# Kernel tuning notes

Hardware: AMD Instinct MI355X
Metric: run time of the kernel (lower is better)

## Reference

```python
import jax, jax.numpy as jnp
import numpy as np

B, N, T, F, D = 2, 8, 128, 128, 256
EPS = 1e-5


def setup_inputs() -> dict:
    key = jax.random.key(0)
    ks = jax.random.split(key, 8)
    s = 1.0 / np.sqrt(D)
    s2 = 1.0 / np.sqrt(2 * D)
    return {
        "x": jax.random.normal(ks[0], (B, N, D), dtype=jnp.float32),
        "t_emb": jax.random.normal(ks[1], (T, D), dtype=jnp.float32),
        "f_emb": jax.random.normal(ks[2], (F, D), dtype=jnp.float32),
        "ln_g": jnp.ones((D,), dtype=jnp.float32),
        "ln_b": jnp.zeros((D,), dtype=jnp.float32),
        "W1": jax.random.uniform(ks[3], (D, 2 * D), jnp.float32, -s, s),
        "b1": jax.random.uniform(ks[4], (2 * D,), jnp.float32, -s, s),
        "W2": jax.random.uniform(ks[5], (2 * D, 2), jnp.float32, -s2, s2),
        "b2": jax.random.uniform(ks[6], (2,), jnp.float32, -s2, s2),
    }


def reference(x, t_emb, f_emb, ln_g, ln_b, W1, b1, W2, b2):
    # x: [B,N,D]; pos_emb: [T,F,D]; broadcast-add -> [B,N,T,F,D]
    pos = t_emb[:, None, :] + f_emb[None, :, :]            # [T,F,D]
    h = x[:, :, None, None, :] + pos[None, None]           # [B,N,T,F,D]
    # LayerNorm over last dim
    mu = jnp.mean(h, axis=-1, keepdims=True)
    var = jnp.mean(jnp.square(h - mu), axis=-1, keepdims=True)
    h = (h - mu) * jax.lax.rsqrt(var + EPS) * ln_g + ln_b
    # MLP: D -> 2D -> 2
    h = jax.nn.relu(jnp.einsum("bntfd,de->bntfe", h, W1) + b1)
    out = jnp.einsum("bntfe,eo->bntfo", h, W2) + b2        # [B,N,T,F,2]
    return out
```

## Files before the change

kernel.cpp:

```cpp
#include <hip/hip_runtime.h>
#include <stdint.h>


#define D_ 256
#define E_ 512

typedef __attribute__((ext_vector_type(8))) short short8;
typedef __attribute__((ext_vector_type(4))) short short4v;
typedef __attribute__((ext_vector_type(4))) float f32x4;
typedef __attribute__((ext_vector_type(2))) float f32x2;

__device__ alignas(16) unsigned short g_Abuf[2176 * 768];
__device__ alignas(16) unsigned short g_Bbuf[768 * 640];
__device__ alignas(16) float g_U[2048 * 512];
__device__ alignas(16) float g_C[2048 * 128];
__device__ alignas(16) float g_Vt[512 * 128];
__device__ alignas(16) float g_GKW[512 * 4];
__device__ alignas(16) float g_sxt[2048];
__device__ alignas(16) float g_sqxt[2048];
__device__ alignas(16) float g_sf[128];
__device__ alignas(16) float g_sqf[128];

__device__ inline unsigned short f2bf(float f) {
  unsigned int u = __float_as_uint(f);
  u += 0x7fffu + ((u >> 16) & 1u);
  return (unsigned short)(u >> 16);
}
__device__ inline float bf2f(unsigned short h) {
  return __uint_as_float(((unsigned int)h) << 16);
}

__global__ __launch_bounds__(256) void prep(
    const float* __restrict__ x, const float* __restrict__ t_emb,
    const float* __restrict__ f_emb, const float* __restrict__ ln_g,
    const float* __restrict__ ln_b, const float* __restrict__ W1,
    const float* __restrict__ b1, const float* __restrict__ W2) {
  __shared__ float sW[32][264];
  __shared__ float sF[128][36];
  __shared__ float sg[32];
  __shared__ float red[4][64][2];

  const int blk = blockIdx.x;
  const int tid = threadIdx.x;
  const int wv = tid >> 6;
  const int l = tid & 63;

  if (blk < 544) {
    int arow;
    float v0, v1, v2, v3;
    if (blk < 512) {
      const int r = blk * 4 + wv;
      const int bn = r >> 7, t = r & 127;
      const float4 xv = *(const float4*)(x + bn * D_ + 4 * l);
      const float4 tv = *(const float4*)(t_emb + t * D_ + 4 * l);
      v0 = xv.x + tv.x; v1 = xv.y + tv.y;
      v2 = xv.z + tv.z; v3 = xv.w + tv.w;
      arow = r;
    } else {
      const int fi = (blk - 512) * 4 + wv;
      const float4 fv = *(const float4*)(f_emb + fi * D_ + 4 * l);
      v0 = fv.x; v1 = fv.y; v2 = fv.z; v3 = fv.w;
      arow = 2048 + fi;
    }
    union { unsigned short u[4]; short4v v; } hi, lo;
    hi.u[0] = f2bf(v0); hi.u[1] = f2bf(v1);
    hi.u[2] = f2bf(v2); hi.u[3] = f2bf(v3);
    lo.u[0] = f2bf(v0 - bf2f(hi.u[0]));
    lo.u[1] = f2bf(v1 - bf2f(hi.u[1]));
    lo.u[2] = f2bf(v2 - bf2f(hi.u[2]));
    lo.u[3] = f2bf(v3 - bf2f(hi.u[3]));
    unsigned short* ab = g_Abuf + arow * 768 + 4 * l;
    *(short4v*)(ab) = hi.v;
    *(short4v*)(ab + 256) = lo.v;
    *(short4v*)(ab + 512) = hi.v;
    float s = (v0 + v1) + (v2 + v3);
    float q = fmaf(v0, v0, fmaf(v1, v1, fmaf(v2, v2, v3 * v3)));
#pragma unroll
    for (int d = 1; d < 64; d <<= 1) {
      s += __shfl_xor(s, d);
      q += __shfl_xor(q, d);
    }
    if (l == 0) {
      if (arow < 2048) { g_sxt[arow] = s; g_sqxt[arow] = q; }
      else             { g_sf[arow - 2048] = s; g_sqf[arow - 2048] = q; }
    }
  } else if (blk < 552) {
    const int e = (blk - 544) * 64 + l;
    const int k0 = wv * 64;
    float G = 0.f, K = 0.f;
#pragma unroll 8
    for (int i = 0; i < 64; ++i) {
      const float wval = W1[(k0 + i) * E_ + e];
      G = fmaf(ln_g[k0 + i], wval, G);
      K = fmaf(ln_b[k0 + i], wval, K);
    }
    red[wv][l][0] = G;
    red[wv][l][1] = K;
    __syncthreads();
    if (wv == 0) {
      G = (red[0][l][0] + red[1][l][0]) + (red[2][l][0] + red[3][l][0]);
      K = (red[0][l][1] + red[1][l][1]) + (red[2][l][1] + red[3][l][1]);
      float4 o;
      o.x = G; o.y = K + b1[e];
      o.z = W2[2 * e]; o.w = W2[2 * e + 1];
      *(float4*)(g_GKW + 4 * e) = o;
    }
  } else {
    const int b = blk - 552;
    const int kt = b >> 1, h = b & 1;
    const int term = kt >> 3;
    const int k0 = (kt & 7) * 32;
    {
      const float4* w4 = (const float4*)(W1 + (size_t)k0 * E_ + h * 256);
      for (int i = tid; i < 2048; i += 256) {
        const int kk2 = i >> 6, c4 = i & 63;
        *(float4*)&sW[kk2][c4 * 4] = w4[kk2 * (E_ / 4) + c4];
      }
      if (tid < 32) sg[tid] = ln_g[k0 + tid];
      if (h == 0) {
        const float4* f4 = (const float4*)(f_emb + k0);
        for (int i = tid; i < 1024; i += 256) {
          const int fr = i >> 3, c4 = i & 7;
          *(float4*)&sF[fr][c4 * 4] = f4[fr * (D_ / 4) + c4];
        }
      }
    }
    __syncthreads();
    for (int fi = tid; fi < 1024; fi += 256) {
      const int ct = 4 * h + (fi >> 8);
      const int rem = fi & 255;
      const int jtl = rem >> 6, ln = rem & 63;
      const int colw = (ct - 4 * h) * 64 + jtl * 16 + (ln & 15);
      const int kb = ((ln >> 4) & 3) * 8;
      union { unsigned short u[8]; short8 v; } fr8;
#pragma unroll
      for (int j = 0; j < 8; ++j) {
        const float v = sg[kb + j] * sW[kb + j][colw];
        const unsigned short hv = f2bf(v);
        fr8.u[j] = (term == 2) ? f2bf(v - bf2f(hv)) : hv;
      }
      const int gidx = ((kt * 10 + ct) * 4 + jtl) * 64 + ln;
      *(short8*)(g_Bbuf + gidx * 8) = fr8.v;
    }
    if (h == 0) {
      for (int fi = tid; fi < 512; fi += 256) {
        const int ct = 8 + (fi >> 8);
        const int rem = fi & 255;
        const int jtl = rem >> 6, ln = rem & 63;
        const int f = (ct - 8) * 64 + jtl * 16 + (ln & 15);
        const int kb = ((ln >> 4) & 3) * 8;
        union { unsigned short u[8]; short8 v; } fr8;
#pragma unroll
        for (int j = 0; j < 8; ++j) {
          const float v = sF[f][kb + j];
          const unsigned short hv = f2bf(v);
          fr8.u[j] = (term == 2) ? f2bf(v - bf2f(hv)) : hv;
        }
        const int gidx = ((kt * 10 + ct) * 4 + jtl) * 64 + ln;
        *(short8*)(g_Bbuf + gidx * 8) = fr8.v;
      }
    }
  }
}

__global__ __launch_bounds__(256) void gemm3() {
  const int tid = threadIdx.x;
  const int wave = tid >> 6, lane = tid & 63;
  const int quad = (lane >> 4) & 3, n16 = lane & 15;
  const int rt = blockIdx.x / 10, ct = blockIdx.x % 10;
  const int rowb = rt * 128 + wave * 32;

  const unsigned short* a0 = g_Abuf + (size_t)(rowb + n16) * 768 + quad * 8;
  const unsigned short* a1 = a0 + 16 * 768;

  f32x4 acc[2][4];
#pragma unroll
  for (int j = 0; j < 4; ++j) {
    acc[0][j] = (f32x4){0.f, 0.f, 0.f, 0.f};
    acc[1][j] = (f32x4){0.f, 0.f, 0.f, 0.f};
  }

#pragma unroll 4
  for (int kt = 0; kt < 24; ++kt) {
    const short8 av0 = *(const short8*)(a0 + kt * 32);
    const short8 av1 = *(const short8*)(a1 + kt * 32);
    const short8* bp = (const short8*)g_Bbuf + ((kt * 10 + ct) * 4) * 64 + lane;
#pragma unroll
    for (int jtl = 0; jtl < 4; ++jtl) {
      const short8 bf = bp[jtl * 64];
      acc[0][jtl] =
          __builtin_amdgcn_mfma_f32_16x16x32_bf16(av0, bf, acc[0][jtl], 0, 0, 0);
      acc[1][jtl] =
          __builtin_amdgcn_mfma_f32_16x16x32_bf16(av1, bf, acc[1][jtl], 0, 0, 0);
    }
  }

#pragma unroll
  for (int g = 0; g < 2; ++g)
#pragma unroll
    for (int jtl = 0; jtl < 4; ++jtl)
#pragma unroll
      for (int r = 0; r < 4; ++r) {
        const float val = acc[g][jtl][r];
        const int grow = rowb + g * 16 + quad * 4 + r;
        const int col = ct * 64 + jtl * 16 + n16;
        if (rt < 16) {
          if (ct < 8) g_U[grow * 512 + col] = val;
          else        g_C[grow * 128 + (col - 512)] = val;
        } else if (ct < 8) {
          g_Vt[col * 128 + (grow - 2048)] = val;
        }
      }
}

__global__ __launch_bounds__(512) void decode2(const float* __restrict__ b2,
                                               float* __restrict__ out) {
  __shared__ float part[8][64][17];
  const int tid = threadIdx.x;
  const int w = tid >> 6, lane = tid & 63;
  const int bnt0 = blockIdx.x * 4;

  const f32x2 sf2 = *(const f32x2*)(g_sf + 2 * lane);
  const f32x2 sqf2 = *(const f32x2*)(g_sqf + 2 * lane);
  f32x2 Ar[4], Br[4];
#pragma unroll
  for (int ti = 0; ti < 4; ++ti) {
    const float sx = g_sxt[bnt0 + ti];
    const float sqx = g_sqxt[bnt0 + ti];
    const f32x2 c2 = *(const f32x2*)(g_C + (bnt0 + ti) * 128 + 2 * lane);
    const f32x2 mu = (sf2 + sx) * (1.0f / 256.0f);
    const f32x2 var = (sqf2 + 2.0f * c2 + sqx) * (1.0f / 256.0f) - mu * mu;
    f32x2 rs;
    rs.x = rsqrtf(var.x + 1e-5f);
    rs.y = rsqrtf(var.y + 1e-5f);
    Ar[ti] = rs;
    Br[ti] = -rs * mu;
  }

  f32x2 o0[4] = {(f32x2){0.f, 0.f}, (f32x2){0.f, 0.f},
                 (f32x2){0.f, 0.f}, (f32x2){0.f, 0.f}};
  f32x2 o1[4] = {(f32x2){0.f, 0.f}, (f32x2){0.f, 0.f},
                 (f32x2){0.f, 0.f}, (f32x2){0.f, 0.f}};
  const int ebase = __builtin_amdgcn_readfirstlane(w * 64);
#pragma unroll 8
  for (int ei = 0; ei < 64; ++ei) {
    const int e = ebase + ei;
    const float4 gkw = *(const float4*)(g_GKW + 4 * e);
    const f32x2 v2 = *(const f32x2*)(g_Vt + e * 128 + 2 * lane);
#pragma unroll
    for (int ti = 0; ti < 4; ++ti) {
      const float u = g_U[(bnt0 + ti) * 512 + e];
      const f32x2 s = v2 + u;
      const f32x2 pre = Ar[ti] * s + (Br[ti] * gkw.x + gkw.y);
      f32x2 y;
      y.x = fmaxf(pre.x, 0.f);
      y.y = fmaxf(pre.y, 0.f);
      o0[ti] += y * gkw.z;
      o1[ti] += y * gkw.w;
    }
  }

#pragma unroll
  for (int ti = 0; ti < 4; ++ti) {
    part[w][lane][ti * 4 + 0] = o0[ti].x;
    part[w][lane][ti * 4 + 1] = o1[ti].x;
    part[w][lane][ti * 4 + 2] = o0[ti].y;
    part[w][lane][ti * 4 + 3] = o1[ti].y;
  }
  __syncthreads();

  const int t = tid >> 7, f = tid & 127;
  const int m = f >> 1, ff = f & 1;
  float r0 = b2[0], r1 = b2[1];
#pragma unroll
  for (int w2 = 0; w2 < 8; ++w2) {
    r0 += part[w2][m][t * 4 + ff * 2 + 0];
    r1 += part[w2][m][t * 4 + ff * 2 + 1];
  }
  float2 res;
  res.x = r0;
  res.y = r1;
  *(float2*)(out + ((bnt0 + t) * 128 + f) * 2) = res;
}

extern "C" void kernel_launch(void* const* d_in, const int* in_sizes, int n_in,
                              void* d_out, int out_size, void* d_ws,
                              size_t ws_size, hipStream_t stream) {
  const float* x = (const float*)d_in[0];
  const float* t_emb = (const float*)d_in[1];
  const float* f_emb = (const float*)d_in[2];
  const float* ln_g = (const float*)d_in[3];
  const float* ln_b = (const float*)d_in[4];
  const float* W1 = (const float*)d_in[5];
  const float* b1 = (const float*)d_in[6];
  const float* W2 = (const float*)d_in[7];
  const float* b2 = (const float*)d_in[8];
  (void)d_ws; (void)ws_size;

  prep<<<600, 256, 0, stream>>>(x, t_emb, f_emb, ln_g, ln_b, W1, b1, W2);
  gemm3<<<170, 256, 0, stream>>>();
  decode2<<<512, 512, 0, stream>>>(b2, (float*)d_out);
}
```

Before: 114.6 us.

## Fuse A-operand bf16 split conversion into GEMM and shrink prep grid

Removes the g_Abuf staging buffer: the GEMM now reads fp32 x/t_emb/f_emb directly, adds x+t on the fly, and builds the hi/lo bf16 split fragments in registers per k-step. The prep kernel drops from 600 to 88 blocks, keeping only the B-operand packing, the GKW reduction, and row-statistics computation with each wave handling 17 rows. This cuts global write/read traffic and launch work in prep, at the cost of extra conversion ALU and redundant fp32 loads inside the GEMM inner loop.

```diff
diff --git a/kernel.cpp b/kernel.cpp
--- a/kernel.cpp
+++ b/kernel.cpp
@@ -6,11 +6,9 @@
 #define E_ 512
 
 typedef __attribute__((ext_vector_type(8))) short short8;
-typedef __attribute__((ext_vector_type(4))) short short4v;
 typedef __attribute__((ext_vector_type(4))) float f32x4;
 typedef __attribute__((ext_vector_type(2))) float f32x2;
 
-__device__ alignas(16) unsigned short g_Abuf[2176 * 768];
 __device__ alignas(16) unsigned short g_Bbuf[768 * 640];
 __device__ alignas(16) float g_U[2048 * 512];
 __device__ alignas(16) float g_C[2048 * 128];
@@ -30,7 +28,18 @@
   return __uint_as_float(((unsigned int)h) << 16);
 }
 
-__global__ __launch_bounds__(256) void prep(
+__device__ inline short8 mk_frag(float4 a0, float4 a1, int term) {
+  union { unsigned short u[8]; short8 v; } fr;
+  float vv[8] = {a0.x, a0.y, a0.z, a0.w, a1.x, a1.y, a1.z, a1.w};
+#pragma unroll
+  for (int j = 0; j < 8; ++j) {
+    const unsigned short h = f2bf(vv[j]);
+    fr.u[j] = (term == 1) ? f2bf(vv[j] - bf2f(h)) : h;
+  }
+  return fr.v;
+}
+
+__global__ __launch_bounds__(256) void prep2(
     const float* __restrict__ x, const float* __restrict__ t_emb,
     const float* __restrict__ f_emb, const float* __restrict__ ln_g,
     const float* __restrict__ ln_b, const float* __restrict__ W1,
@@ -45,47 +54,63 @@
   const int wv = tid >> 6;
   const int l = tid & 63;
 
-  if (blk < 544) {
-    int arow;
-    float v0, v1, v2, v3;
-    if (blk < 512) {
-      const int r = blk * 4 + wv;
-      const int bn = r >> 7, t = r & 127;
-      const float4 xv = *(const float4*)(x + bn * D_ + 4 * l);
-      const float4 tv = *(const float4*)(t_emb + t * D_ + 4 * l);
-      v0 = xv.x + tv.x; v1 = xv.y + tv.y;
-      v2 = xv.z + tv.z; v3 = xv.w + tv.w;
-      arow = r;
-    } else {
-      const int fi = (blk - 512) * 4 + wv;
-      const float4 fv = *(const float4*)(f_emb + fi * D_ + 4 * l);
-      v0 = fv.x; v1 = fv.y; v2 = fv.z; v3 = fv.w;
-      arow = 2048 + fi;
-    }
-    union { unsigned short u[4]; short4v v; } hi, lo;
-    hi.u[0] = f2bf(v0); hi.u[1] = f2bf(v1);
-    hi.u[2] = f2bf(v2); hi.u[3] = f2bf(v3);
-    lo.u[0] = f2bf(v0 - bf2f(hi.u[0]));
-    lo.u[1] = f2bf(v1 - bf2f(hi.u[1]));
-    lo.u[2] = f2bf(v2 - bf2f(hi.u[2]));
-    lo.u[3] = f2bf(v3 - bf2f(hi.u[3]));
-    unsigned short* ab = g_Abuf + arow * 768 + 4 * l;
-    *(short4v*)(ab) = hi.v;
-    *(short4v*)(ab + 256) = lo.v;
-    *(short4v*)(ab + 512) = hi.v;
-    float s = (v0 + v1) + (v2 + v3);
-    float q = fmaf(v0, v0, fmaf(v1, v1, fmaf(v2, v2, v3 * v3)));
-#pragma unroll
-    for (int d = 1; d < 64; d <<= 1) {
-      s += __shfl_xor(s, d);
-      q += __shfl_xor(q, d);
-    }
-    if (l == 0) {
-      if (arow < 2048) { g_sxt[arow] = s; g_sqxt[arow] = q; }
-      else             { g_sf[arow - 2048] = s; g_sqf[arow - 2048] = q; }
-    }
-  } else if (blk < 552) {
-    const int e = (blk - 544) * 64 + l;
+  if (blk < 48) {
+    const int b = blk;
+    const int kt = b >> 1, h = b & 1;
+    const int term = kt >> 3;
+    const int k0 = (kt & 7) * 32;
+    {
+      const float4* w4 = (const float4*)(W1 + (size_t)k0 * E_ + h * 256);
+      for (int i = tid; i < 2048; i += 256) {
+        const int kk2 = i >> 6, c4 = i & 63;
+        *(float4*)&sW[kk2][c4 * 4] = w4[kk2 * (E_ / 4) + c4];
+      }
+      if (tid < 32) sg[tid] = ln_g[k0 + tid];
+      if (h == 0) {
+        const float4* f4 = (const float4*)(f_emb + k0);
+        for (int i = tid; i < 1024; i += 256) {
+          const int fr = i >> 3, c4 = i & 7;
+          *(float4*)&sF[fr][c4 * 4] = f4[fr * (D_ / 4) + c4];
+        }
+      }
+    }
+    __syncthreads();
+    for (int fi = tid; fi < 1024; fi += 256) {
+      const int ct = 4 * h + (fi >> 8);
+      const int rem = fi & 255;
+      const int jtl = rem >> 6, ln = rem & 63;
+      const int colw = (ct - 4 * h) * 64 + jtl * 16 + (ln & 15);
+      const int kb = ((ln >> 4) & 3) * 8;
+      union { unsigned short u[8]; short8 v; } fr8;
+#pragma unroll
+      for (int j = 0; j < 8; ++j) {
+        const float v = sg[kb + j] * sW[kb + j][colw];
+        const unsigned short hv = f2bf(v);
+        fr8.u[j] = (term == 2) ? f2bf(v - bf2f(hv)) : hv;
+      }
+      const int gidx = ((kt * 10 + ct) * 4 + jtl) * 64 + ln;
+      *(short8*)(g_Bbuf + gidx * 8) = fr8.v;
+    }
+    if (h == 0) {
+      for (int fi = tid; fi < 512; fi += 256) {
+        const int ct = 8 + (fi >> 8);
+        const int rem = fi & 255;
+        const int jtl = rem >> 6, ln = rem & 63;
+        const int f = (ct - 8) * 64 + jtl * 16 + (ln & 15);
+        const int kb = ((ln >> 4) & 3) * 8;
+        union { unsigned short u[8]; short8 v; } fr8;
+#pragma unroll
+        for (int j = 0; j < 8; ++j) {
+          const float v = sF[f][kb + j];
+          const unsigned short hv = f2bf(v);
+          fr8.u[j] = (term == 2) ? f2bf(v - bf2f(hv)) : hv;
+        }
+        const int gidx = ((kt * 10 + ct) * 4 + jtl) * 64 + ln;
+        *(short8*)(g_Bbuf + gidx * 8) = fr8.v;
+      }
+    }
+  } else if (blk < 56) {
+    const int e = (blk - 48) * 64 + l;
     const int k0 = wv * 64;
     float G = 0.f, K = 0.f;
 #pragma unroll 8
@@ -106,72 +131,56 @@
       *(float4*)(g_GKW + 4 * e) = o;
     }
   } else {
-    const int b = blk - 552;
-    const int kt = b >> 1, h = b & 1;
-    const int term = kt >> 3;
-    const int k0 = (kt & 7) * 32;
-    {
-      const float4* w4 = (const float4*)(W1 + (size_t)k0 * E_ + h * 256);
-      for (int i = tid; i < 2048; i += 256) {
-        const int kk2 = i >> 6, c4 = i & 63;
-        *(float4*)&sW[kk2][c4 * 4] = w4[kk2 * (E_ / 4) + c4];
-      }
-      if (tid < 32) sg[tid] = ln_g[k0 + tid];
-      if (h == 0) {
-        const float4* f4 = (const float4*)(f_emb + k0);
-        for (int i = tid; i < 1024; i += 256) {
-          const int fr = i >> 3, c4 = i & 7;
-          *(float4*)&sF[fr][c4 * 4] = f4[fr * (D_ / 4) + c4];
-        }
-      }
-    }
-    __syncthreads();
-    for (int fi = tid; fi < 1024; fi += 256) {
-      const int ct = 4 * h + (fi >> 8);
-      const int rem = fi & 255;
-      const int jtl = rem >> 6, ln = rem & 63;
-      const int colw = (ct - 4 * h) * 64 + jtl * 16 + (ln & 15);
-      const int kb = ((ln >> 4) & 3) * 8;
-      union { unsigned short u[8]; short8 v; } fr8;
-#pragma unroll
-      for (int j = 0; j < 8; ++j) {
-        const float v = sg[kb + j] * sW[kb + j][colw];
-        const unsigned short hv = f2bf(v);
-        fr8.u[j] = (term == 2) ? f2bf(v - bf2f(hv)) : hv;
-      }
-      const int gidx = ((kt * 10 + ct) * 4 + jtl) * 64 + ln;
-      *(short8*)(g_Bbuf + gidx * 8) = fr8.v;
-    }
-    if (h == 0) {
-      for (int fi = tid; fi < 512; fi += 256) {
-        const int ct = 8 + (fi >> 8);
-        const int rem = fi & 255;
-        const int jtl = rem >> 6, ln = rem & 63;
-        const int f = (ct - 8) * 64 + jtl * 16 + (ln & 15);
-        const int kb = ((ln >> 4) & 3) * 8;
-        union { unsigned short u[8]; short8 v; } fr8;
-#pragma unroll
-        for (int j = 0; j < 8; ++j) {
-          const float v = sF[f][kb + j];
-          const unsigned short hv = f2bf(v);
-          fr8.u[j] = (term == 2) ? f2bf(v - bf2f(hv)) : hv;
-        }
-        const int gidx = ((kt * 10 + ct) * 4 + jtl) * 64 + ln;
-        *(short8*)(g_Bbuf + gidx * 8) = fr8.v;
-      }
-    }
-  }
-}
-
-__global__ __launch_bounds__(256) void gemm3() {
+    const int w0 = ((blk - 56) * 4 + wv) * 17;
+    for (int i = 0; i < 17; ++i) {
+      const int r = w0 + i;
+      float v0, v1, v2, v3;
+      if (r < 2048) {
+        const int bn = r >> 7, t = r & 127;
+        const float4 xv = *(const float4*)(x + bn * D_ + 4 * l);
+        const float4 tv = *(const float4*)(t_emb + t * D_ + 4 * l);
+        v0 = xv.x + tv.x; v1 = xv.y + tv.y;
+        v2 = xv.z + tv.z; v3 = xv.w + tv.w;
+      } else {
+        const float4 fv = *(const float4*)(f_emb + (r - 2048) * D_ + 4 * l);
+        v0 = fv.x; v1 = fv.y; v2 = fv.z; v3 = fv.w;
+      }
+      float s = (v0 + v1) + (v2 + v3);
+      float q = fmaf(v0, v0, fmaf(v1, v1, fmaf(v2, v2, v3 * v3)));
+#pragma unroll
+      for (int d = 1; d < 64; d <<= 1) {
+        s += __shfl_xor(s, d);
+        q += __shfl_xor(q, d);
+      }
+      if (l == 0) {
+        if (r < 2048) { g_sxt[r] = s; g_sqxt[r] = q; }
+        else          { g_sf[r - 2048] = s; g_sqf[r - 2048] = q; }
+      }
+    }
+  }
+}
+
+__global__ __launch_bounds__(256) void gemm3b(const float* __restrict__ x,
+                                              const float* __restrict__ t_emb,
+                                              const float* __restrict__ f_emb) {
   const int tid = threadIdx.x;
   const int wave = tid >> 6, lane = tid & 63;
   const int quad = (lane >> 4) & 3, n16 = lane & 15;
   const int rt = blockIdx.x / 10, ct = blockIdx.x % 10;
   const int rowb = rt * 128 + wave * 32;
 
-  const unsigned short* a0 = g_Abuf + (size_t)(rowb + n16) * 768 + quad * 8;
-  const unsigned short* a1 = a0 + 16 * 768;
+  const float* base0;
+  const float* base1;
+  const float* xrow;
+  if (rt < 16) {
+    base0 = t_emb + (size_t)(wave * 32 + n16) * D_;
+    base1 = base0 + 16 * D_;
+    xrow = x + (size_t)rt * D_;
+  } else {
+    base0 = f_emb + (size_t)(wave * 32 + n16) * D_;
+    base1 = base0 + 16 * D_;
+    xrow = nullptr;
+  }
 
   f32x4 acc[2][4];
 #pragma unroll
@@ -182,8 +191,22 @@
 
 #pragma unroll 4
   for (int kt = 0; kt < 24; ++kt) {
-    const short8 av0 = *(const short8*)(a0 + kt * 32);
-    const short8 av1 = *(const short8*)(a1 + kt * 32);
+    const int term = kt >> 3;
+    const int kb = (kt & 7) * 32 + quad * 8;
+    float4 t0a = *(const float4*)(base0 + kb);
+    float4 t0b = *(const float4*)(base0 + kb + 4);
+    float4 t1a = *(const float4*)(base1 + kb);
+    float4 t1b = *(const float4*)(base1 + kb + 4);
+    if (rt < 16) {
+      const float4 xa = *(const float4*)(xrow + kb);
+      const float4 xb = *(const float4*)(xrow + kb + 4);
+      t0a.x += xa.x; t0a.y += xa.y; t0a.z += xa.z; t0a.w += xa.w;
+      t0b.x += xb.x; t0b.y += xb.y; t0b.z += xb.z; t0b.w += xb.w;
+      t1a.x += xa.x; t1a.y += xa.y; t1a.z += xa.z; t1a.w += xa.w;
+      t1b.x += xb.x; t1b.y += xb.y; t1b.z += xb.z; t1b.w += xb.w;
+    }
+    const short8 av0 = mk_frag(t0a, t0b, term);
+    const short8 av1 = mk_frag(t1a, t1b, term);
     const short8* bp = (const short8*)g_Bbuf + ((kt * 10 + ct) * 4) * 64 + lane;
 #pragma unroll
     for (int jtl = 0; jtl < 4; ++jtl) {
@@ -297,7 +320,7 @@
   const float* b2 = (const float*)d_in[8];
   (void)d_ws; (void)ws_size;
 
-  prep<<<600, 256, 0, stream>>>(x, t_emb, f_emb, ln_g, ln_b, W1, b1, W2);
-  gemm3<<<170, 256, 0, stream>>>();
+  prep2<<<88, 256, 0, stream>>>(x, t_emb, f_emb, ln_g, ln_b, W1, b1, W2);
+  gemm3b<<<170, 256, 0, stream>>>(x, t_emb, f_emb);
   decode2<<<512, 512, 0, stream>>>(b2, (float*)d_out);
 }
```

Result: slower. 128.5 us (+12.1%).
